# Optimization experiments

Measured on AMD Instinct MI355X. Metric: run time of the kernel, lower is better.

The kernel has to match this reference:

```python
import jax, jax.numpy as jnp
import numpy as np

B, C, H, W = 16, 256, 64, 64
NH = 4                      # num_heads
HD = C // NH                # head_dim = 64
G = 32                      # GroupNorm groups
EPS = 1e-5


def setup_inputs() -> dict:
    key = jax.random.key(0)
    ks = jax.random.split(key, 7)
    x = jax.random.normal(ks[0], (B, C, H, W), dtype=jnp.float32)
    gn_w = jnp.ones((C,), dtype=jnp.float32)
    gn_b = jnp.zeros((C,), dtype=jnp.float32)
    qkv_w = jax.random.normal(ks[1], (3 * C, C), dtype=jnp.float32) * 0.02
    qkv_b = jnp.zeros((3 * C,), dtype=jnp.float32)
    out_w = jax.random.normal(ks[2], (C, C), dtype=jnp.float32) * 0.02
    out_b = jnp.zeros((C,), dtype=jnp.float32)
    return {"x": x, "gn_w": gn_w, "gn_b": gn_b, "qkv_w": qkv_w,
            "qkv_b": qkv_b, "out_w": out_w, "out_b": out_b}


def _group_norm(x, w, b):
    # x: (B, C, H, W); normalize over each of G groups of channels (+ spatial)
    Bx, Cx, Hx, Wx = x.shape
    xr = x.reshape(Bx, G, -1)
    mean = xr.mean(axis=-1, keepdims=True)
    var = xr.var(axis=-1, keepdims=True)
    h = ((xr - mean) * jax.lax.rsqrt(var + EPS)).reshape(Bx, Cx, Hx, Wx)
    return h * w[None, :, None, None] + b[None, :, None, None]


def reference(x, gn_w, gn_b, qkv_w, qkv_b, out_w, out_b):
    Bx, Cx, Hx, Wx = x.shape
    N = Hx * Wx
    h = _group_norm(x, gn_w, gn_b)
    # 1x1 conv == channel matmul
    qkv = jnp.einsum('oc,bchw->bohw', qkv_w, h) + qkv_b[None, :, None, None]
    q, k, v = jnp.split(qkv, 3, axis=1)
    # b (h d) y x -> b h d n
    q = q.reshape(Bx, NH, HD, N)
    k = k.reshape(Bx, NH, HD, N)
    v = v.reshape(Bx, NH, HD, N)
    q = jax.nn.softmax(q, axis=-1)   # over spatial positions n
    k = jax.nn.softmax(k, axis=-2)   # over head_dim d
    # context = k @ v^T : (b,h,d,d)
    context = jnp.einsum('bhdn,bhen->bhde', k, v)
    # out = context^T @ q : (b,h,d,n)
    out = jnp.einsum('bhde,bhdn->bhen', context, q)
    out = out.reshape(Bx, Cx, Hx, Wx)
    out = jnp.einsum('oc,bchw->bohw', out_w, out) + out_b[None, :, None, None]
    return x + out
```

## Files before the change

kernel.cpp:

```cpp
#include <hip/hip_runtime.h>


typedef __bf16 bf16x8 __attribute__((ext_vector_type(8)));
typedef __bf16 bf16x4 __attribute__((ext_vector_type(4)));
typedef float  f32x4  __attribute__((ext_vector_type(4)));

__device__ __forceinline__ float wave_red_sum(float v) {
#pragma unroll
    for (int off = 32; off > 0; off >>= 1) v += __shfl_xor(v, off, 64);
    return v;
}
__device__ __forceinline__ float wave_red_max(float v) {
#pragma unroll
    for (int off = 32; off > 0; off >>= 1) v = fmaxf(v, __shfl_xor(v, off, 64));
    return v;
}

__global__ __launch_bounds__(256)
void gn_stats_kernel(const float* __restrict__ x, const float* __restrict__ gw,
                     const float* __restrict__ gb, float2* __restrict__ scsh)
{
    const int blk = blockIdx.x;
    const int b = blk >> 5, g = blk & 31;
    const int tid = threadIdx.x;
    const int lane = tid & 63, wid = tid >> 6;
    const size_t xbase = ((size_t)(b * 256 + g * 8)) * 4096;

    float s1 = 0.f, s2 = 0.f;
#pragma unroll
    for (int it = 0; it < 32; it++) {
        const int idx = (it * 256 + tid) * 4;
        const float4 v4 = *(const float4*)(x + xbase + idx);
        s1 += v4.x + v4.y + v4.z + v4.w;
        s2 += v4.x * v4.x + v4.y * v4.y + v4.z * v4.z + v4.w * v4.w;
    }
    __shared__ float red[8];
    float s1w = wave_red_sum(s1);
    float s2w = wave_red_sum(s2);
    if (lane == 0) { red[wid] = s1w; red[4 + wid] = s2w; }
    __syncthreads();
    const float mean = (red[0] + red[1] + red[2] + red[3]) * (1.0f / 32768.0f);
    const float ms   = (red[4] + red[5] + red[6] + red[7]) * (1.0f / 32768.0f);
    const float inv  = rsqrtf(fmaxf(ms - mean * mean, 0.f) + 1e-5f);

    if (tid < 8) {
        const int c = g * 8 + tid;
        const float sc = gw[c] * inv;
        const float sh = gb[c] - mean * sc;
        scsh[b * 256 + c] = make_float2(sc, sh);
    }
}

__global__ __launch_bounds__(256)
void wcast_kernel(const float* __restrict__ w, __bf16* __restrict__ wb)
{
    const int i = (blockIdx.x * 256 + threadIdx.x) * 4;
    const float4 f = *(const float4*)(w + i);
    bf16x4 t;
    t[0] = (__bf16)f.x; t[1] = (__bf16)f.y; t[2] = (__bf16)f.z; t[3] = (__bf16)f.w;
    *(bf16x4*)(wb + i) = t;
}

__global__ __launch_bounds__(256)
void gemm1_kernel(const __bf16* __restrict__ wbf,
                  const float* __restrict__ x,
                  const float* __restrict__ bias,
                  const float2* __restrict__ scsh,
                  __bf16* __restrict__ qkv)
{
    __shared__ __align__(16) char lds_a[8192];
    __shared__ __align__(16) char lds_b[8192];
    __shared__ float2 lscsh[256];

    const int tid  = threadIdx.x;
    const int lane = tid & 63;
    const int wid  = tid >> 6;
    const int quad = lane >> 4;
    const int tcol = lane & 15;
    const int wm   = (wid & 1) * 64;
    const int wn   = (wid >> 1) * 64;
    const int n0   = blockIdx.x * 128;
    const int m0   = blockIdx.y * 128;
    const int b    = n0 >> 12;
    const int nn   = n0 & 4095;

    lscsh[tid] = scsh[b * 256 + tid];

    const int sn  = tid & 127;
    const int sth = tid >> 7;
    const int am  = tid >> 1;
    const int ah  = tid & 1;

    f32x4 acc[4][4];
#pragma unroll
    for (int i = 0; i < 4; i++)
#pragma unroll
        for (int j = 0; j < 4; j++) acc[i][j] = {0.f, 0.f, 0.f, 0.f};

    const float* xcol = x + (size_t)b * 1048576 + nn + sn;
    const int aswz = (am >> 1) & 3;
    const int bswz = (sn >> 1) & 3;

    for (int kt = 0; kt < 256; kt += 32) {
        __syncthreads();
        {
            const __bf16* asrc = wbf + (m0 + am) * 256 + kt + ah * 16;
            const bf16x8 a0 = *(const bf16x8*)asrc;
            const bf16x8 a1 = *(const bf16x8*)(asrc + 8);
            *(bf16x8*)&lds_a[am * 64 + (((ah * 2)     + aswz) & 3) * 16] = a0;
            *(bf16x8*)&lds_a[am * 64 + (((ah * 2 + 1) + aswz) & 3) * 16] = a1;
        }
        {
            const float* xs = xcol + (size_t)(kt + sth * 16) * 4096;
            bf16x8 o0, o1;
#pragma unroll
            for (int j = 0; j < 16; j++) {
                const float2 ss = lscsh[kt + sth * 16 + j];
                const float f = xs[(size_t)j * 4096];
                const __bf16 v = (__bf16)(f * ss.x + ss.y);
                if (j < 8) o0[j] = v; else o1[j - 8] = v;
            }
            *(bf16x8*)&lds_b[sn * 64 + (((sth * 2)     + bswz) & 3) * 16] = o0;
            *(bf16x8*)&lds_b[sn * 64 + (((sth * 2 + 1) + bswz) & 3) * 16] = o1;
        }
        __syncthreads();

        bf16x8 af[4], bfr[4];
#pragma unroll
        for (int mi = 0; mi < 4; mi++) {
            const int m = wm + mi * 16 + tcol;
            af[mi] = *(const bf16x8*)&lds_a[m * 64 + ((quad + ((m >> 1) & 3)) & 3) * 16];
        }
#pragma unroll
        for (int ni = 0; ni < 4; ni++) {
            const int n = wn + ni * 16 + tcol;
            bfr[ni] = *(const bf16x8*)&lds_b[n * 64 + ((quad + ((n >> 1) & 3)) & 3) * 16];
        }
#pragma unroll
        for (int mi = 0; mi < 4; mi++)
#pragma unroll
            for (int ni = 0; ni < 4; ni++)
                acc[mi][ni] = __builtin_amdgcn_mfma_f32_16x16x32_bf16(
                    af[mi], bfr[ni], acc[mi][ni], 0, 0, 0);
    }

#pragma unroll
    for (int mi = 0; mi < 4; mi++) {
#pragma unroll
        for (int r = 0; r < 4; r++) {
            const int grow = m0 + wm + mi * 16 + quad * 4 + r;
            const float bv = bias[grow];
#pragma unroll
            for (int ni = 0; ni < 4; ni++) {
                const int gcol = n0 + wn + ni * 16 + tcol;
                qkv[(size_t)grow * 65536 + gcol] = (__bf16)(acc[mi][ni][r] + bv);
            }
        }
    }
}

__global__ __launch_bounds__(256)
void qstats_kernel(const __bf16* __restrict__ qkv, float2* __restrict__ qst)
{
    const int o = blockIdx.x >> 4;
    const int b = blockIdx.x & 15;
    const int tid = threadIdx.x;
    const int lane = tid & 63, wid = tid >> 6;
    const size_t base = (size_t)o * 65536 + (size_t)b * 4096;

    float v[16];
    float m = -INFINITY;
#pragma unroll
    for (int s = 0; s < 16; s++) {
        v[s] = (float)qkv[base + s * 256 + tid];
        m = fmaxf(m, v[s]);
    }
    __shared__ float red[4];
    float wmx = wave_red_max(m);
    if (lane == 0) red[wid] = wmx;
    __syncthreads();
    m = fmaxf(fmaxf(red[0], red[1]), fmaxf(red[2], red[3]));
    __syncthreads();
    float sum = 0.f;
#pragma unroll
    for (int s = 0; s < 16; s++) sum += __expf(v[s] - m);
    float wsm = wave_red_sum(sum);
    if (lane == 0) red[wid] = wsm;
    __syncthreads();
    if (tid == 0)
        qst[o * 16 + b] = make_float2(m, 1.0f / (red[0] + red[1] + red[2] + red[3]));
}

__global__ __launch_bounds__(256)
void ctx_mfma_kernel(const __bf16* __restrict__ qkv, float* __restrict__ ctx)
{
    const int bh = blockIdx.x >> 3, kc = blockIdx.x & 7;
    const int b = bh >> 2, hh = bh & 3;
    __shared__ __align__(16) __bf16 lk[64 * 72], lv[64 * 72];
    __shared__ float smax[4][64], ssum[4][64];
    const int tid = threadIdx.x;
    const int lane = tid & 63, wid = tid >> 6;
    const int quad = lane >> 4, tcol = lane & 15;
    const int eh = (wid & 1) * 32, dh = (wid >> 1) * 32;
    const int col = tid & 63, dq = tid >> 6;
    const int sd = tid >> 2, snn = (tid & 3) * 16;

    f32x4 acc[2][2];
#pragma unroll
    for (int i = 0; i < 2; i++)
#pragma unroll
        for (int j = 0; j < 2; j++) acc[i][j] = {0.f, 0.f, 0.f, 0.f};

    const size_t kbase = (size_t)(256 + hh * 64) * 65536 + (size_t)b * 4096 + kc * 512;
    const size_t vbase = (size_t)(512 + hh * 64) * 65536 + (size_t)b * 4096 + kc * 512;

    for (int nc = 0; nc < 512; nc += 64) {
        __syncthreads();
        {
            const __bf16* ks = qkv + kbase + (size_t)sd * 65536 + nc + snn;
            *(bf16x8*)&lk[sd * 72 + snn]     = *(const bf16x8*)ks;
            *(bf16x8*)&lk[sd * 72 + snn + 8] = *(const bf16x8*)(ks + 8);
            const __bf16* vs = qkv + vbase + (size_t)sd * 65536 + nc + snn;
            *(bf16x8*)&lv[sd * 72 + snn]     = *(const bf16x8*)vs;
            *(bf16x8*)&lv[sd * 72 + snn + 8] = *(const bf16x8*)(vs + 8);
        }
        __syncthreads();

        float kvv[16];
        float pm = -INFINITY;
#pragma unroll
        for (int i = 0; i < 16; i++) {
            kvv[i] = (float)lk[(dq * 16 + i) * 72 + col];
            pm = fmaxf(pm, kvv[i]);
        }
        smax[dq][col] = pm;
        __syncthreads();
        const float m = fmaxf(fmaxf(smax[0][col], smax[1][col]),
                              fmaxf(smax[2][col], smax[3][col]));
        float ps = 0.f;
#pragma unroll
        for (int i = 0; i < 16; i++) { kvv[i] = __expf(kvv[i] - m); ps += kvv[i]; }
        ssum[dq][col] = ps;
        __syncthreads();
        const float inv = 1.0f / (ssum[0][col] + ssum[1][col] + ssum[2][col] + ssum[3][col]);
#pragma unroll
        for (int i = 0; i < 16; i++)
            lk[(dq * 16 + i) * 72 + col] = (__bf16)(kvv[i] * inv);
        __syncthreads();

#pragma unroll
        for (int k2 = 0; k2 < 64; k2 += 32) {
            bf16x8 af[2], bfr[2];
#pragma unroll
            for (int mi = 0; mi < 2; mi++)
                af[mi] = *(const bf16x8*)&lv[(eh + mi * 16 + tcol) * 72 + k2 + quad * 8];
#pragma unroll
            for (int ni = 0; ni < 2; ni++)
                bfr[ni] = *(const bf16x8*)&lk[(dh + ni * 16 + tcol) * 72 + k2 + quad * 8];
#pragma unroll
            for (int mi = 0; mi < 2; mi++)
#pragma unroll
                for (int ni = 0; ni < 2; ni++)
                    acc[mi][ni] = __builtin_amdgcn_mfma_f32_16x16x32_bf16(
                        af[mi], bfr[ni], acc[mi][ni], 0, 0, 0);
        }
    }
    float* cb = ctx + (size_t)bh * 4096;
#pragma unroll
    for (int mi = 0; mi < 2; mi++)
#pragma unroll
        for (int ni = 0; ni < 2; ni++)
#pragma unroll
            for (int r = 0; r < 4; r++) {
                const int e = eh + mi * 16 + quad * 4 + r;
                const int d = dh + ni * 16 + tcol;
                atomicAdd(&cb[e * 64 + d], acc[mi][ni][r]);
            }
}

__global__ __launch_bounds__(256)
void w2_kernel(const float* __restrict__ ctx, const float* __restrict__ out_w,
               __bf16* __restrict__ w2)
{
    const int bh = blockIdx.x;
    const int b = bh >> 2, hh = bh & 3;
    const int tid = threadIdx.x;

    __shared__ __align__(16) float lctx[4096];
    const float* csrc = ctx + (size_t)bh * 4096;
#pragma unroll
    for (int i = 0; i < 4; i++)
        ((float4*)lctx)[tid + i * 256] = ((const float4*)csrc)[tid + i * 256];
    __syncthreads();

    float acc[64];
#pragma unroll
    for (int d = 0; d < 64; d++) acc[d] = 0.f;

    const float* wrow = out_w + (size_t)tid * 256 + hh * 64;
    for (int e = 0; e < 64; e++) {
        const float w = wrow[e];
#pragma unroll
        for (int d4 = 0; d4 < 64; d4 += 4) {
            const float4 c4 = *(const float4*)&lctx[e * 64 + d4];
            acc[d4 + 0] += w * c4.x;
            acc[d4 + 1] += w * c4.y;
            acc[d4 + 2] += w * c4.z;
            acc[d4 + 3] += w * c4.w;
        }
    }
    __bf16* dst = w2 + (size_t)b * 65536 + (size_t)tid * 256 + hh * 64;
#pragma unroll
    for (int d4 = 0; d4 < 64; d4 += 4) {
        bf16x4 t;
        t[0] = (__bf16)acc[d4 + 0]; t[1] = (__bf16)acc[d4 + 1];
        t[2] = (__bf16)acc[d4 + 2]; t[3] = (__bf16)acc[d4 + 3];
        *(bf16x4*)(dst + d4) = t;
    }
}

__global__ __launch_bounds__(256)
void gemm2_kernel(const __bf16* __restrict__ w2,
                  const __bf16* __restrict__ qkv,
                  const float2* __restrict__ qst,
                  const float* __restrict__ bias,
                  const float* __restrict__ xres,
                  float* __restrict__ out)
{
    __shared__ __align__(16) __bf16 lds_bt[128 * 264];
    __shared__ __align__(16) __bf16 lds_a[128 * 40];
    __shared__ float2 lqst[256];

    const int tid  = threadIdx.x;
    const int lane = tid & 63;
    const int wid  = tid >> 6;
    const int quad = lane >> 4;
    const int tcol = lane & 15;
    const int wm   = (wid & 1) * 64;
    const int wn   = (wid >> 1) * 64;
    const int n0   = blockIdx.x * 128;
    const int b    = n0 >> 12;

    lqst[tid] = qst[tid * 16 + b];
    __syncthreads();

    const int sn    = tid & 127;
    const int chalf = tid >> 7;
    const int swz   = (sn >> 3) & 3;
#pragma unroll
    for (int iter = 0; iter < 8; iter++) {
        const int cbase = iter * 32 + chalf * 16;
        bf16x8 o0, o1;
        const __bf16* qs = qkv + n0 + sn;
#pragma unroll
        for (int j = 0; j < 16; j++) {
            const int c = cbase + j;
            const float2 qq = lqst[c];
            const float f = (float)qs[(size_t)c * 65536];
            const __bf16 v = (__bf16)(__expf(f - qq.x) * qq.y);
            if (j < 8) o0[j] = v; else o1[j - 8] = v;
        }
        const int chunk = iter * 2 + chalf;
        const int chSw  = chunk ^ swz;
        __bf16* dst = &lds_bt[sn * 264 + chSw * 16];
        *(bf16x8*)dst       = o0;
        *(bf16x8*)(dst + 8) = o1;
    }

    const int arow = tid >> 1, k16 = (tid & 1) * 16;

    for (int mt = 0; mt < 2; mt++) {
        const int m0 = mt * 128;
        f32x4 acc[4][4];
#pragma unroll
        for (int i = 0; i < 4; i++)
#pragma unroll
            for (int j = 0; j < 4; j++) acc[i][j] = {0.f, 0.f, 0.f, 0.f};

        for (int kt = 0; kt < 256; kt += 32) {
            __syncthreads();
            {
                const __bf16* src = w2 + (size_t)b * 65536
                                  + (size_t)(m0 + arow) * 256 + kt + k16;
                const bf16x8 o0 = *(const bf16x8*)(src);
                const bf16x8 o1 = *(const bf16x8*)(src + 8);
                *(bf16x8*)&lds_a[arow * 40 + k16]     = o0;
                *(bf16x8*)&lds_a[arow * 40 + k16 + 8] = o1;
            }
            __syncthreads();

            bf16x8 af[4];
#pragma unroll
            for (int mi = 0; mi < 4; mi++)
                af[mi] = *(const bf16x8*)&lds_a[(wm + mi * 16 + tcol) * 40 + quad * 8];
            bf16x8 bfr[4];
#pragma unroll
            for (int ni = 0; ni < 4; ni++) {
                const int n = wn + ni * 16 + tcol;
                const int k = kt + quad * 8;
                const int chSw = (k >> 4) ^ ((n >> 3) & 3);
                bfr[ni] = *(const bf16x8*)&lds_bt[n * 264 + chSw * 16 + (k & 15)];
            }
#pragma unroll
            for (int mi = 0; mi < 4; mi++)
#pragma unroll
                for (int ni = 0; ni < 4; ni++)
                    acc[mi][ni] = __builtin_amdgcn_mfma_f32_16x16x32_bf16(
                        af[mi], bfr[ni], acc[mi][ni], 0, 0, 0);
        }

#pragma unroll
        for (int mi = 0; mi < 4; mi++) {
#pragma unroll
            for (int r = 0; r < 4; r++) {
                const int grow = m0 + wm + mi * 16 + quad * 4 + r;
                const float bv = bias[grow];
#pragma unroll
                for (int ni = 0; ni < 4; ni++) {
                    const int gcol = n0 + wn + ni * 16 + tcol;
                    const int n = gcol & 4095;
                    const size_t oidx = ((size_t)(b * 256 + grow)) * 4096 + n;
                    out[oidx] = acc[mi][ni][r] + bv + xres[oidx];
                }
            }
        }
    }
}

extern "C" void kernel_launch(void* const* d_in, const int* in_sizes, int n_in,
                              void* d_out, int out_size, void* d_ws, size_t ws_size,
                              hipStream_t stream)
{
    const float* x     = (const float*)d_in[0];
    const float* gn_w  = (const float*)d_in[1];
    const float* gn_b  = (const float*)d_in[2];
    const float* qkv_w = (const float*)d_in[3];
    const float* qkv_b = (const float*)d_in[4];
    const float* out_w = (const float*)d_in[5];
    const float* out_b = (const float*)d_in[6];
    float* out = (float*)d_out;

    char* ws = (char*)d_ws;
    __bf16* qkv  = (__bf16*)ws;
    float*  ctx  = (float*)(ws + (size_t)100663296);
    float2* scsh = (float2*)(ws + (size_t)101711872);
    float2* qst  = (float2*)(ws + (size_t)101744640);
    __bf16* wbf  = (__bf16*)(ws + (size_t)101777408);
    __bf16* w2   = qkv + (size_t)256 * 65536;

    hipMemsetAsync(ctx, 0, 262144 * sizeof(float), stream);
    gn_stats_kernel<<<512, 256, 0, stream>>>(x, gn_w, gn_b, scsh);
    wcast_kernel<<<192, 256, 0, stream>>>(qkv_w, wbf);
    gemm1_kernel<<<dim3(512, 6), 256, 0, stream>>>(wbf, x, qkv_b, scsh, qkv);
    qstats_kernel<<<4096, 256, 0, stream>>>(qkv, qst);
    ctx_mfma_kernel<<<512, 256, 0, stream>>>(qkv, ctx);
    w2_kernel<<<64, 256, 0, stream>>>(ctx, out_w, w2);
    gemm2_kernel<<<512, 256, 0, stream>>>(w2, qkv, qst, out_b, x, out);
}
```

Measured before the change: 281.1 us.

## Keep normalized x tile resident in LDS across all output tiles in gemm1

gemm1 now launches one block per 128-column spatial tile. Each block normalizes the full 256-channel slab of x once into a padded, swizzled LDS buffer, then loops over all six 128-row weight tiles, register-prefetching the next A slice. Before, six separate blocks each re-read and re-normalized the same x columns. The weight cast kernel is also folded into gn_stats to remove one launch. In exchange, the grid shrinks from 3072 to 512 blocks and LDS use grows to about 78KB per block, which lowers occupancy and parallelism.

```diff
diff --git a/kernel.cpp b/kernel.cpp
--- a/kernel.cpp
+++ b/kernel.cpp
@@ -3,6 +3,7 @@
 
 typedef __bf16 bf16x8 __attribute__((ext_vector_type(8)));
 typedef __bf16 bf16x4 __attribute__((ext_vector_type(4)));
+typedef __bf16 bf16x2 __attribute__((ext_vector_type(2)));
 typedef float  f32x4  __attribute__((ext_vector_type(4)));
 
 __device__ __forceinline__ float wave_red_sum(float v) {
@@ -18,7 +19,8 @@
 
 __global__ __launch_bounds__(256)
 void gn_stats_kernel(const float* __restrict__ x, const float* __restrict__ gw,
-                     const float* __restrict__ gb, float2* __restrict__ scsh)
+                     const float* __restrict__ gb, const float* __restrict__ qw,
+                     float2* __restrict__ scsh, __bf16* __restrict__ wb)
 {
     const int blk = blockIdx.x;
     const int b = blk >> 5, g = blk & 31;
@@ -26,6 +28,15 @@
     const int lane = tid & 63, wid = tid >> 6;
     const size_t xbase = ((size_t)(b * 256 + g * 8)) * 4096;
 
+    {
+        const int ci = (blk * 256 + tid) * 2;
+        if (ci < 196608) {
+            const float2 f = *(const float2*)(qw + ci);
+            bf16x2 t; t[0] = (__bf16)f.x; t[1] = (__bf16)f.y;
+            *(bf16x2*)(wb + ci) = t;
+        }
+    }
+
     float s1 = 0.f, s2 = 0.f;
 #pragma unroll
     for (int it = 0; it < 32; it++) {
@@ -52,24 +63,14 @@
 }
 
 __global__ __launch_bounds__(256)
-void wcast_kernel(const float* __restrict__ w, __bf16* __restrict__ wb)
-{
-    const int i = (blockIdx.x * 256 + threadIdx.x) * 4;
-    const float4 f = *(const float4*)(w + i);
-    bf16x4 t;
-    t[0] = (__bf16)f.x; t[1] = (__bf16)f.y; t[2] = (__bf16)f.z; t[3] = (__bf16)f.w;
-    *(bf16x4*)(wb + i) = t;
-}
-
-__global__ __launch_bounds__(256)
 void gemm1_kernel(const __bf16* __restrict__ wbf,
                   const float* __restrict__ x,
                   const float* __restrict__ bias,
                   const float2* __restrict__ scsh,
                   __bf16* __restrict__ qkv)
 {
-    __shared__ __align__(16) char lds_a[8192];
-    __shared__ __align__(16) char lds_b[8192];
+    __shared__ __align__(16) __bf16 lds_bt[128 * 264];
+    __shared__ __align__(16) __bf16 lds_a[128 * 40];
     __shared__ float2 lscsh[256];
 
     const int tid  = threadIdx.x;
@@ -80,80 +81,92 @@
     const int wm   = (wid & 1) * 64;
     const int wn   = (wid >> 1) * 64;
     const int n0   = blockIdx.x * 128;
-    const int m0   = blockIdx.y * 128;
     const int b    = n0 >> 12;
     const int nn   = n0 & 4095;
 
     lscsh[tid] = scsh[b * 256 + tid];
-
-    const int sn  = tid & 127;
-    const int sth = tid >> 7;
-    const int am  = tid >> 1;
-    const int ah  = tid & 1;
-
-    f32x4 acc[4][4];
-#pragma unroll
-    for (int i = 0; i < 4; i++)
-#pragma unroll
-        for (int j = 0; j < 4; j++) acc[i][j] = {0.f, 0.f, 0.f, 0.f};
-
-    const float* xcol = x + (size_t)b * 1048576 + nn + sn;
-    const int aswz = (am >> 1) & 3;
-    const int bswz = (sn >> 1) & 3;
-
-    for (int kt = 0; kt < 256; kt += 32) {
-        __syncthreads();
-        {
-            const __bf16* asrc = wbf + (m0 + am) * 256 + kt + ah * 16;
-            const bf16x8 a0 = *(const bf16x8*)asrc;
-            const bf16x8 a1 = *(const bf16x8*)(asrc + 8);
-            *(bf16x8*)&lds_a[am * 64 + (((ah * 2)     + aswz) & 3) * 16] = a0;
-            *(bf16x8*)&lds_a[am * 64 + (((ah * 2 + 1) + aswz) & 3) * 16] = a1;
-        }
-        {
-            const float* xs = xcol + (size_t)(kt + sth * 16) * 4096;
-            bf16x8 o0, o1;
-#pragma unroll
-            for (int j = 0; j < 16; j++) {
-                const float2 ss = lscsh[kt + sth * 16 + j];
-                const float f = xs[(size_t)j * 4096];
-                const __bf16 v = (__bf16)(f * ss.x + ss.y);
-                if (j < 8) o0[j] = v; else o1[j - 8] = v;
-            }
-            *(bf16x8*)&lds_b[sn * 64 + (((sth * 2)     + bswz) & 3) * 16] = o0;
-            *(bf16x8*)&lds_b[sn * 64 + (((sth * 2 + 1) + bswz) & 3) * 16] = o1;
-        }
-        __syncthreads();
-
-        bf16x8 af[4], bfr[4];
+    __syncthreads();
+
+    const int sn    = tid & 127;
+    const int chalf = tid >> 7;
+    const int swz   = (sn >> 3) & 3;
+    const float* xs = x + (size_t)b * 1048576 + nn + sn;
+#pragma unroll
+    for (int iter = 0; iter < 8; iter++) {
+        const int cbase = iter * 32 + chalf * 16;
+        bf16x8 o0, o1;
+#pragma unroll
+        for (int j = 0; j < 16; j++) {
+            const int c = cbase + j;
+            const float2 ss = lscsh[c];
+            const float f = xs[(size_t)c * 4096];
+            const __bf16 v = (__bf16)(f * ss.x + ss.y);
+            if (j < 8) o0[j] = v; else o1[j - 8] = v;
+        }
+        const int chunk = iter * 2 + chalf;
+        const int chSw  = chunk ^ swz;
+        __bf16* dst = &lds_bt[sn * 264 + chSw * 16];
+        *(bf16x8*)dst       = o0;
+        *(bf16x8*)(dst + 8) = o1;
+    }
+
+    const int arow = tid >> 1, k16 = (tid & 1) * 16;
+    const __bf16* asrc0 = wbf + (size_t)arow * 256 + k16;
+
+    for (int mt = 0; mt < 6; mt++) {
+        const int m0 = mt * 128;
+        f32x4 acc[4][4];
+#pragma unroll
+        for (int i = 0; i < 4; i++)
+#pragma unroll
+            for (int j = 0; j < 4; j++) acc[i][j] = {0.f, 0.f, 0.f, 0.f};
+
+        const __bf16* asrc = asrc0 + (size_t)m0 * 256;
+        bf16x8 a0 = *(const bf16x8*)(asrc);
+        bf16x8 a1 = *(const bf16x8*)(asrc + 8);
+
+        for (int kt = 0; kt < 256; kt += 32) {
+            __syncthreads();
+            *(bf16x8*)&lds_a[arow * 40 + k16]     = a0;
+            *(bf16x8*)&lds_a[arow * 40 + k16 + 8] = a1;
+            if (kt < 224) {
+                const __bf16* an = asrc + kt + 32;
+                a0 = *(const bf16x8*)(an);
+                a1 = *(const bf16x8*)(an + 8);
+            }
+            __syncthreads();
+
+            bf16x8 af[4];
+#pragma unroll
+            for (int mi = 0; mi < 4; mi++)
+                af[mi] = *(const bf16x8*)&lds_a[(wm + mi * 16 + tcol) * 40 + quad * 8];
+            bf16x8 bfr[4];
+#pragma unroll
+            for (int ni = 0; ni < 4; ni++) {
+                const int n = wn + ni * 16 + tcol;
+                const int k = kt + quad * 8;
+                const int chSw2 = (k >> 4) ^ ((n >> 3) & 3);
+                bfr[ni] = *(const bf16x8*)&lds_bt[n * 264 + chSw2 * 16 + (k & 15)];
+            }
+#pragma unroll
+            for (int mi = 0; mi < 4; mi++)
+#pragma unroll
+                for (int ni = 0; ni < 4; ni++)
+                    acc[mi][ni] = __builtin_amdgcn_mfma_f32_16x16x32_bf16(
+                        af[mi], bfr[ni], acc[mi][ni], 0, 0, 0);
+        }
+
 #pragma unroll
         for (int mi = 0; mi < 4; mi++) {
-            const int m = wm + mi * 16 + tcol;
-            af[mi] = *(const bf16x8*)&lds_a[m * 64 + ((quad + ((m >> 1) & 3)) & 3) * 16];
-        }
-#pragma unroll
-        for (int ni = 0; ni < 4; ni++) {
-            const int n = wn + ni * 16 + tcol;
-            bfr[ni] = *(const bf16x8*)&lds_b[n * 64 + ((quad + ((n >> 1) & 3)) & 3) * 16];
-        }
-#pragma unroll
-        for (int mi = 0; mi < 4; mi++)
-#pragma unroll
-            for (int ni = 0; ni < 4; ni++)
-                acc[mi][ni] = __builtin_amdgcn_mfma_f32_16x16x32_bf16(
-                    af[mi], bfr[ni], acc[mi][ni], 0, 0, 0);
-    }
-
-#pragma unroll
-    for (int mi = 0; mi < 4; mi++) {
-#pragma unroll
-        for (int r = 0; r < 4; r++) {
-            const int grow = m0 + wm + mi * 16 + quad * 4 + r;
-            const float bv = bias[grow];
-#pragma unroll
-            for (int ni = 0; ni < 4; ni++) {
-                const int gcol = n0 + wn + ni * 16 + tcol;
-                qkv[(size_t)grow * 65536 + gcol] = (__bf16)(acc[mi][ni][r] + bv);
+#pragma unroll
+            for (int r = 0; r < 4; r++) {
+                const int grow = m0 + wm + mi * 16 + quad * 4 + r;
+                const float bv = bias[grow];
+#pragma unroll
+                for (int ni = 0; ni < 4; ni++) {
+                    const int gcol = n0 + wn + ni * 16 + tcol;
+                    qkv[(size_t)grow * 65536 + gcol] = (__bf16)(acc[mi][ni][r] + bv);
+                }
             }
         }
     }
@@ -449,9 +462,8 @@
     __bf16* w2   = qkv + (size_t)256 * 65536;
 
     hipMemsetAsync(ctx, 0, 262144 * sizeof(float), stream);
-    gn_stats_kernel<<<512, 256, 0, stream>>>(x, gn_w, gn_b, scsh);
-    wcast_kernel<<<192, 256, 0, stream>>>(qkv_w, wbf);
-    gemm1_kernel<<<dim3(512, 6), 256, 0, stream>>>(wbf, x, qkv_b, scsh, qkv);
+    gn_stats_kernel<<<512, 256, 0, stream>>>(x, gn_w, gn_b, qkv_w, scsh, wbf);
+    gemm1_kernel<<<512, 256, 0, stream>>>(wbf, x, qkv_b, scsh, qkv);
     qstats_kernel<<<4096, 256, 0, stream>>>(qkv, qst);
     ctx_mfma_kernel<<<512, 256, 0, stream>>>(qkv, ctx);
     w2_kernel<<<64, 256, 0, stream>>>(ctx, out_w, w2);
```

Result: faster. 255.1 us (-9.3%).
